# Optimization experiments

Measured on AMD Instinct MI355X. Metric: run time of the kernel, lower is better.

Reference implementation:

```python
import jax, jax.numpy as jnp
import numpy as np

B, T = 128, 32
E, H, L, V = 512, 512, 256, 16000


def setup_inputs() -> dict:
    key = jax.random.key(0)
    ks = jax.random.split(key, 12)
    u = lambda k, shape, s: jax.random.uniform(k, shape, jnp.float32, -s, s)
    kH = float(1.0 / np.sqrt(H))
    return {
        "features": jax.random.normal(ks[0], (B, E), jnp.float32),
        "captions": jax.random.randint(ks[1], (B, T), 0, V, dtype=jnp.int32),
        "lengths": jnp.full((B,), T, dtype=jnp.int32),
        "noise": jax.random.normal(ks[2], (B, T, L), jnp.float32),
        "embed_W": u(ks[3], (V, E), 0.1),
        "W_ih": u(ks[4], (4 * H, E + L), kH),
        "W_hh": u(ks[5], (4 * H, H), kH),
        "b_ih": u(ks[6], (4 * H,), kH),
        "b_hh": u(ks[7], (4 * H,), kH),
        "qz_W": u(ks[8], (2 * L, E + H), 0.1),
        "qz_b": jnp.zeros((2 * L,), jnp.float32),
        "prior_W": u(ks[9], (2 * L, H), 0.1),
        "prior_b": jnp.zeros((2 * L,), jnp.float32),
        "qx_W": u(ks[10], (V, L + H), 0.1),
        "qx_b": jnp.zeros((V,), jnp.float32),
    }


def reference(features, captions, lengths, noise, embed_W, W_ih, W_hh, b_ih, b_hh,
              qz_W, qz_b, prior_W, prior_b, qx_W, qx_b):
    def lstm_step(h, c, x):
        # PyTorch gate order: i, f, g, o
        gates = x @ W_ih.T + h @ W_hh.T + (b_ih + b_hh)
        i, f, g, o = jnp.split(gates, 4, axis=1)
        c_new = jax.nn.sigmoid(f) * c + jax.nn.sigmoid(i) * jnp.tanh(g)
        return jax.nn.sigmoid(o) * jnp.tanh(c_new), c_new

    # initial LSTM step on [features, z_0=0]
    x0 = jnp.concatenate([features, jnp.zeros((B, L), features.dtype)], axis=1)
    h, c = lstm_step(jnp.zeros((B, H), features.dtype), jnp.zeros((B, H), features.dtype), x0)

    emb = embed_W[captions]                # [B, T, E]
    emb_t = jnp.swapaxes(emb, 0, 1)        # [T, B, E]
    eps_t = jnp.swapaxes(noise, 0, 1)      # [T, B, L]

    def step(carry, xs):
        h, c = carry
        e_t, n_t = xs
        p = h @ prior_W.T + prior_b
        p_mu, p_sigma = jnp.split(p, 2, axis=1)
        q = jnp.concatenate([e_t, h], axis=1) @ qz_W.T + qz_b
        q_mu, q_sigma = jnp.split(q, 2, axis=1)
        z = n_t * q_sigma + q_mu
        logits = jnp.concatenate([z, h], axis=1) @ qx_W.T + qx_b
        q_x = jax.nn.log_softmax(logits, axis=1)
        h, c = lstm_step(h, c, jnp.concatenate([e_t, z], axis=1))
        return (h, c), (p_mu, p_sigma, q_mu, q_sigma, q_x)

    _, outs = jax.lax.scan(step, (h, c), (emb_t, eps_t))
    # pack_padded_sequence with equal lengths == time-major flatten: [T, B, D] -> [T*B, D]
    p_mus, p_sigmas, q_mus, q_sigmas, q_xs = [o.reshape((-1,) + o.shape[2:]) for o in outs]
    return ((p_mus, p_sigmas), (q_mus, q_sigmas), q_xs)
```

## Files before the change

kernel.cpp:

```cpp
#include <hip/hip_runtime.h>
#include <hip/hip_bf16.h>

typedef short bf16v8 __attribute__((ext_vector_type(8)));
typedef float f32x4 __attribute__((ext_vector_type(4)));


__device__ __forceinline__ void gload16(const void* g, void* l) {
    __builtin_amdgcn_global_load_lds(
        (const __attribute__((address_space(1))) void*)g,
        (__attribute__((address_space(3))) void*)l,
        16, 0, 0);
}

template<int SPLIT>
__global__ __launch_bounds__(256, 2) void gemm_bt(
    const __hip_bfloat16* __restrict__ A, int ldA,
    const __hip_bfloat16* __restrict__ B, int ldB,
    float* __restrict__ C, int ldC, float* __restrict__ C2,
    const float* __restrict__ bias,
    int K, int nTilesN)
{
    __shared__ __hip_bfloat16 As[128 * 32];
    __shared__ __hip_bfloat16 Bs[128 * 32];
    const int bid = blockIdx.x;
    const int bm = bid / nTilesN, bn = bid % nTilesN;
    const int m0 = bm * 128, n0 = bn * 128;
    const int tid = threadIdx.x, lane = tid & 63, wave = tid >> 6;
    const int wm = (wave & 1) * 64, wn = (wave >> 1) * 64;
    f32x4 acc[4][4] = {};

    const int ci0 = wave, ci1 = wave + 4;
    const int srow0 = ci0 * 16 + (lane >> 2);
    const int srow1 = ci1 * 16 + (lane >> 2);
    const int scol = (lane & 3) * 8;
    const __hip_bfloat16* Ag0 = A + (size_t)(m0 + srow0) * ldA + scol;
    const __hip_bfloat16* Ag1 = A + (size_t)(m0 + srow1) * ldA + scol;
    const __hip_bfloat16* Bg0 = B + (size_t)(n0 + srow0) * ldB + scol;
    const __hip_bfloat16* Bg1 = B + (size_t)(n0 + srow1) * ldB + scol;
    char* AsB = (char*)As;
    char* BsB = (char*)Bs;
    const int fr = lane & 15, k0 = (lane >> 4) * 8;

    for (int kt = 0; kt < K; kt += 32) {
        gload16(Ag0 + kt, AsB + ci0 * 1024);
        gload16(Ag1 + kt, AsB + ci1 * 1024);
        gload16(Bg0 + kt, BsB + ci0 * 1024);
        gload16(Bg1 + kt, BsB + ci1 * 1024);
        __syncthreads();
        bf16v8 a[4], b[4];
        #pragma unroll
        for (int mi = 0; mi < 4; ++mi)
            a[mi] = *(const bf16v8*)(AsB + ((wm + mi * 16 + fr) * 32 + k0) * 2);
        #pragma unroll
        for (int ni = 0; ni < 4; ++ni)
            b[ni] = *(const bf16v8*)(BsB + ((wn + ni * 16 + fr) * 32 + k0) * 2);
        #pragma unroll
        for (int mi = 0; mi < 4; ++mi)
            #pragma unroll
            for (int ni = 0; ni < 4; ++ni)
                acc[mi][ni] = __builtin_amdgcn_mfma_f32_16x16x32_bf16(a[mi], b[ni], acc[mi][ni], 0, 0, 0);
        __syncthreads();
    }
    #pragma unroll
    for (int ni = 0; ni < 4; ++ni) {
        const int n = n0 + wn + ni * 16 + fr;
        const float bv = bias ? bias[n] : 0.f;
        #pragma unroll
        for (int mi = 0; mi < 4; ++mi) {
            #pragma unroll
            for (int r = 0; r < 4; ++r) {
                const int m = m0 + wm + mi * 16 + (lane >> 4) * 4 + r;
                const float v = acc[mi][ni][r] + bv;
                if (SPLIT) {
                    if (n < 256) C[(size_t)m * 256 + n] = v;
                    else         C2[(size_t)m * 256 + (n - 256)] = v;
                } else {
                    C[(size_t)m * ldC + n] = v;
                }
            }
        }
    }
}

__global__ __launch_bounds__(256) void qz_step_k(
    const float* __restrict__ h,
    const float* __restrict__ Qe_t,
    const float* __restrict__ qz_W,
    const float* __restrict__ qz_b,
    const float* __restrict__ noise,
    float* __restrict__ out_qmu_t,
    float* __restrict__ out_qsig_t,
    float* __restrict__ zf,
    __hip_bfloat16* __restrict__ XH_z,
    int t)
{
    __shared__ float2 Wms[64][33];
    __shared__ float xt[8][32];
    const int rt = (int)blockIdx.x >> 2, nt = (int)blockIdx.x & 3;
    const int r0 = rt * 8, n0 = nt * 64;
    const int tid = threadIdx.x, lane = tid & 63, wave = tid >> 6;
    float accm[2] = {0.f, 0.f}, accs[2] = {0.f, 0.f};
    for (int kt = 0; kt < 512; kt += 32) {
        #pragma unroll
        for (int j = 0; j < 8; ++j) {
            int e = tid + j * 256, nl = e >> 5, kl = e & 31;
            size_t col = 512 + kt + kl;
            Wms[nl][kl] = make_float2(qz_W[(size_t)(n0 + nl) * 1024 + col],
                                      qz_W[(size_t)(n0 + nl + 256) * 1024 + col]);
        }
        { int rl = tid >> 5, kl = tid & 31;
          xt[rl][kl] = h[(size_t)(r0 + rl) * 512 + kt + kl]; }
        __syncthreads();
        #pragma unroll 8
        for (int kk = 0; kk < 32; ++kk) {
            float2 w = Wms[lane][kk];
            #pragma unroll
            for (int i = 0; i < 2; ++i) {
                float hv = xt[wave * 2 + i][kk];
                accm[i] = fmaf(hv, w.x, accm[i]);
                accs[i] = fmaf(hv, w.y, accs[i]);
            }
        }
        __syncthreads();
    }
    const int c = n0 + lane;
    const float bm = qz_b[c], bs = qz_b[c + 256];
    #pragma unroll
    for (int i = 0; i < 2; ++i) {
        const int b = r0 + wave * 2 + i;
        float qm = accm[i] + Qe_t[(size_t)b * 512 + c] + bm;
        float qs = accs[i] + Qe_t[(size_t)b * 512 + c + 256] + bs;
        float nz = noise[((size_t)b * 32 + t) * 256 + c];
        float z = fmaf(nz, qs, qm);
        out_qmu_t[(size_t)b * 256 + c] = qm;
        out_qsig_t[(size_t)b * 256 + c] = qs;
        zf[(size_t)b * 256 + c] = z;
        XH_z[(size_t)b * 768 + c] = __float2bfloat16(z);
    }
}

template<bool INIT>
__global__ __launch_bounds__(256) void lstm_step_k(
    const float* __restrict__ xz, const float* __restrict__ hin,
    const float* __restrict__ cin,
    const float* __restrict__ W_ih, const float* __restrict__ W_hh,
    const float* __restrict__ b_ih, const float* __restrict__ b_hh,
    const float* __restrict__ Ge,
    float* __restrict__ hout, float* __restrict__ cout,
    __hip_bfloat16* __restrict__ XH_h)
{
    __shared__ float4 Wt4[64][33];
    __shared__ float xt[8][32];
    const int rt = (int)blockIdx.x >> 3, jt = (int)blockIdx.x & 7;
    const int r0 = rt * 8, j0 = jt * 64;
    const int tid = threadIdx.x, lane = tid & 63, wave = tid >> 6;
    float acc[4][2] = {};
    const int Kz = INIT ? 512 : 256;
    const int koff = INIT ? 0 : 512;
    for (int kt = 0; kt < Kz; kt += 32) {
        #pragma unroll
        for (int j = 0; j < 8; ++j) {
            int e = tid + j * 256, nl = e >> 5, kl = e & 31;
            size_t col = (size_t)koff + kt + kl;
            Wt4[nl][kl] = make_float4(
                W_ih[(size_t)(j0 + nl) * 768 + col],
                W_ih[(size_t)(j0 + nl + 512) * 768 + col],
                W_ih[(size_t)(j0 + nl + 1024) * 768 + col],
                W_ih[(size_t)(j0 + nl + 1536) * 768 + col]);
        }
        { int rl = tid >> 5, kl = tid & 31;
          xt[rl][kl] = xz[(size_t)(r0 + rl) * Kz + kt + kl]; }
        __syncthreads();
        #pragma unroll 8
        for (int kk = 0; kk < 32; ++kk) {
            float4 w = Wt4[lane][kk];
            #pragma unroll
            for (int i = 0; i < 2; ++i) {
                float xv = xt[wave * 2 + i][kk];
                acc[0][i] = fmaf(xv, w.x, acc[0][i]);
                acc[1][i] = fmaf(xv, w.y, acc[1][i]);
                acc[2][i] = fmaf(xv, w.z, acc[2][i]);
                acc[3][i] = fmaf(xv, w.w, acc[3][i]);
            }
        }
        __syncthreads();
    }
    if constexpr (!INIT) {
        for (int kt = 0; kt < 512; kt += 32) {
            #pragma unroll
            for (int j = 0; j < 8; ++j) {
                int e = tid + j * 256, nl = e >> 5, kl = e & 31;
                size_t col = (size_t)kt + kl;
                Wt4[nl][kl] = make_float4(
                    W_hh[(size_t)(j0 + nl) * 512 + col],
                    W_hh[(size_t)(j0 + nl + 512) * 512 + col],
                    W_hh[(size_t)(j0 + nl + 1024) * 512 + col],
                    W_hh[(size_t)(j0 + nl + 1536) * 512 + col]);
            }
            { int rl = tid >> 5, kl = tid & 31;
              xt[rl][kl] = hin[(size_t)(r0 + rl) * 512 + kt + kl]; }
            __syncthreads();
            #pragma unroll 8
            for (int kk = 0; kk < 32; ++kk) {
                float4 w = Wt4[lane][kk];
                #pragma unroll
                for (int i = 0; i < 2; ++i) {
                    float xv = xt[wave * 2 + i][kk];
                    acc[0][i] = fmaf(xv, w.x, acc[0][i]);
                    acc[1][i] = fmaf(xv, w.y, acc[1][i]);
                    acc[2][i] = fmaf(xv, w.z, acc[2][i]);
                    acc[3][i] = fmaf(xv, w.w, acc[3][i]);
                }
            }
            __syncthreads();
        }
    }
    const int jj = j0 + lane;
    #pragma unroll
    for (int i = 0; i < 2; ++i) {
        const int b = r0 + wave * 2 + i;
        float g0 = acc[0][i] + b_ih[jj] + b_hh[jj];
        float g1 = acc[1][i] + b_ih[jj + 512] + b_hh[jj + 512];
        float g2 = acc[2][i] + b_ih[jj + 1024] + b_hh[jj + 1024];
        float g3 = acc[3][i] + b_ih[jj + 1536] + b_hh[jj + 1536];
        if constexpr (!INIT) {
            const float* ge = Ge + (size_t)b * 2048;
            g0 += ge[jj]; g1 += ge[jj + 512]; g2 += ge[jj + 1024]; g3 += ge[jj + 1536];
        }
        float si = 1.f / (1.f + __expf(-g0));
        float sf = 1.f / (1.f + __expf(-g1));
        float tg = tanhf(g2);
        float so = 1.f / (1.f + __expf(-g3));
        float cold = INIT ? 0.f : cin[(size_t)b * 512 + jj];
        float cn = sf * cold + si * tg;
        float hn = so * tanhf(cn);
        cout[(size_t)b * 512 + jj] = cn;
        hout[(size_t)b * 512 + jj] = hn;
        XH_h[(size_t)b * 768 + jj] = __float2bfloat16(hn);
    }
}

__global__ void embed_k(const float* __restrict__ embW, const int* __restrict__ cap,
                        __hip_bfloat16* __restrict__ Emb) {
    const int row = blockIdx.x;
    const int t = row >> 7, b = row & 127;
    const int tok = cap[b * 32 + t];
    const float* src = embW + (size_t)tok * 512;
    __hip_bfloat16* dst = Emb + (size_t)row * 512;
    for (int k = threadIdx.x; k < 512; k += blockDim.x)
        dst[k] = __float2bfloat16(src[k]);
}

__global__ void conv_lin_k(const float* __restrict__ s, __hip_bfloat16* __restrict__ d, int n) {
    for (int i = blockIdx.x * blockDim.x + threadIdx.x; i < n; i += gridDim.x * blockDim.x)
        d[i] = __float2bfloat16(s[i]);
}

__global__ void conv_s512_k(const float* __restrict__ s, int ld, __hip_bfloat16* __restrict__ d, int n) {
    for (int i = blockIdx.x * blockDim.x + threadIdx.x; i < n; i += gridDim.x * blockDim.x) {
        int r = i >> 9, c = i & 511;
        d[i] = __float2bfloat16(s[(size_t)r * ld + c]);
    }
}

__global__ __launch_bounds__(256) void lse_k(float* __restrict__ logits) {
    __shared__ float buf[16000];
    __shared__ float red[4];
    const int row = blockIdx.x;
    const int tid = threadIdx.x;
    float* p = logits + (size_t)row * 16000;
    float mx = -3.4e38f;
    for (int i = tid; i < 16000; i += 256) { float v = p[i]; buf[i] = v; mx = fmaxf(mx, v); }
    #pragma unroll
    for (int o = 32; o; o >>= 1) mx = fmaxf(mx, __shfl_xor(mx, o));
    if ((tid & 63) == 0) red[tid >> 6] = mx;
    __syncthreads();
    mx = fmaxf(fmaxf(red[0], red[1]), fmaxf(red[2], red[3]));
    float s = 0.f;
    for (int i = tid; i < 16000; i += 256) s += __expf(buf[i] - mx);
    #pragma unroll
    for (int o = 32; o; o >>= 1) s += __shfl_xor(s, o);
    __syncthreads();
    if ((tid & 63) == 0) red[tid >> 6] = s;
    __syncthreads();
    const float lse = mx + logf(red[0] + red[1] + red[2] + red[3]);
    for (int i = tid; i < 16000; i += 256) p[i] = buf[i] - lse;
}

extern "C" void kernel_launch(void* const* d_in, const int* in_sizes, int n_in,
                              void* d_out, int out_size, void* d_ws, size_t ws_size,
                              hipStream_t stream) {
    const float* features = (const float*)d_in[0];
    const int*   captions = (const int*)d_in[1];
    const float* noise    = (const float*)d_in[3];
    const float* embed_W  = (const float*)d_in[4];
    const float* W_ih     = (const float*)d_in[5];
    const float* W_hh     = (const float*)d_in[6];
    const float* b_ih     = (const float*)d_in[7];
    const float* b_hh     = (const float*)d_in[8];
    const float* qz_W     = (const float*)d_in[9];
    const float* qz_b     = (const float*)d_in[10];
    const float* prior_W  = (const float*)d_in[11];
    const float* prior_b  = (const float*)d_in[12];
    const float* qx_W     = (const float*)d_in[13];
    const float* qx_b     = (const float*)d_in[14];

    float* out0 = (float*)d_out;
    float* out1 = out0 + 4096 * 256;
    float* out2 = out1 + 4096 * 256;
    float* out3 = out2 + 4096 * 256;
    float* out4 = out3 + 4096 * 256;

    char* ws = (char*)d_ws;
    __hip_bfloat16* qxWb  = (__hip_bfloat16*)(ws + 0);
    __hip_bfloat16* Emb   = (__hip_bfloat16*)(ws + 24576000);
    __hip_bfloat16* WihEb = (__hip_bfloat16*)(ws + 28770304);
    __hip_bfloat16* qzWEb = (__hip_bfloat16*)(ws + 30867456);
    __hip_bfloat16* priWb = (__hip_bfloat16*)(ws + 31391744);
    __hip_bfloat16* XH    = (__hip_bfloat16*)(ws + 31916032);
    float* Ge  = (float*)(ws + 38404096);
    float* Qe  = (float*)(ws + 71958528);
    float* hb0 = (float*)(ws + 80347136);
    float* hb1 = (float*)(ws + 80609280);
    float* cb0 = (float*)(ws + 80871424);
    float* cb1 = (float*)(ws + 81133568);
    float* zf  = (float*)(ws + 81395712);

    conv_lin_k<<<2048, 256, 0, stream>>>(qx_W, qxWb, 16000 * 768);
    conv_lin_k<<<256, 256, 0, stream>>>(prior_W, priWb, 512 * 512);
    conv_s512_k<<<1024, 256, 0, stream>>>(W_ih, 768, WihEb, 2048 * 512);
    conv_s512_k<<<256, 256, 0, stream>>>(qz_W, 1024, qzWEb, 512 * 512);
    embed_k<<<4096, 256, 0, stream>>>(embed_W, captions, Emb);

    gemm_bt<0><<<512, 256, 0, stream>>>(Emb, 512, WihEb, 512, Ge, 2048, nullptr, nullptr, 512, 16);
    gemm_bt<0><<<128, 256, 0, stream>>>(Emb, 512, qzWEb, 512, Qe, 512, nullptr, nullptr, 512, 4);

    lstm_step_k<true><<<128, 256, 0, stream>>>(features, nullptr, nullptr, W_ih, W_hh,
                                               b_ih, b_hh, nullptr, hb0, cb0, XH + 256);

    for (int t = 0; t < 32; ++t) {
        float* hcur = (t & 1) ? hb1 : hb0;
        float* hnxt = (t & 1) ? hb0 : hb1;
        float* ccur = (t & 1) ? cb1 : cb0;
        float* cnxt = (t & 1) ? cb0 : cb1;
        qz_step_k<<<64, 256, 0, stream>>>(hcur, Qe + (size_t)t * 128 * 512, qz_W, qz_b, noise,
                                          out2 + (size_t)t * 128 * 256,
                                          out3 + (size_t)t * 128 * 256,
                                          zf, XH + (size_t)t * 128 * 768, t);
        lstm_step_k<false><<<128, 256, 0, stream>>>(zf, hcur, ccur, W_ih, W_hh, b_ih, b_hh,
                                                    Ge + (size_t)t * 128 * 2048, hnxt, cnxt,
                                                    XH + (size_t)(t + 1) * 128 * 768 + 256);
    }

    gemm_bt<1><<<128, 256, 0, stream>>>(XH + 256, 768, priWb, 512, out0, 256, out1, prior_b, 512, 4);
    gemm_bt<0><<<4000, 256, 0, stream>>>(XH, 768, qxWb, 768, out4, 16000, nullptr, qx_b, 768, 125);
    lse_k<<<4096, 256, 0, stream>>>(out4);
}
```

Measured before the change: 3.039 ms.

## Run recurrent qz and LSTM steps as bf16 MFMA GEMMs with fused epilogues

Replaces the fp32 scalar-FMA per-step qz and LSTM kernels with a bf16 MFMA GEMM kernel. Its epilogue computes z, and the LSTM gates and cell update, directly from interleaved weight rows that are prepared once up front. Biases are folded into the precomputed embedding GEMMs, and Ge is staged in the logits output buffer to save workspace. The log-softmax kernel is rewritten to hold each row in registers with 1024 threads and float4 accesses, and the qx GEMM grid is rounded to 128 N tiles with an early exit past the last column. The cost is that the recurrent state now passes through bf16, which may shift accuracy, and each step launches only 4 or 16 blocks.

```diff
diff --git a/kernel.cpp b/kernel.cpp
--- a/kernel.cpp
+++ b/kernel.cpp
@@ -11,6 +11,8 @@
         (__attribute__((address_space(3))) void*)l,
         16, 0, 0);
 }
+
+__device__ __forceinline__ float sigm(float x) { return 1.f / (1.f + __expf(-x)); }
 
 template<int SPLIT>
 __global__ __launch_bounds__(256, 2) void gemm_bt(
@@ -18,13 +20,14 @@
     const __hip_bfloat16* __restrict__ B, int ldB,
     float* __restrict__ C, int ldC, float* __restrict__ C2,
     const float* __restrict__ bias,
-    int K, int nTilesN)
+    int K, int nTilesN, int nMax)
 {
     __shared__ __hip_bfloat16 As[128 * 32];
     __shared__ __hip_bfloat16 Bs[128 * 32];
     const int bid = blockIdx.x;
     const int bm = bid / nTilesN, bn = bid % nTilesN;
     const int m0 = bm * 128, n0 = bn * 128;
+    if (n0 >= nMax) return;
     const int tid = threadIdx.x, lane = tid & 63, wave = tid >> 6;
     const int wm = (wave & 1) * 64, wn = (wave >> 1) * 64;
     f32x4 acc[4][4] = {};
@@ -82,162 +85,139 @@
     }
 }
 
-__global__ __launch_bounds__(256) void qz_step_k(
-    const float* __restrict__ h,
-    const float* __restrict__ Qe_t,
-    const float* __restrict__ qz_W,
-    const float* __restrict__ qz_b,
-    const float* __restrict__ noise,
-    float* __restrict__ out_qmu_t,
-    float* __restrict__ out_qsig_t,
-    float* __restrict__ zf,
-    __hip_bfloat16* __restrict__ XH_z,
-    int t)
+template<int EPI, bool INIT>
+__global__ __launch_bounds__(256, 2) void rec_gemm(
+    const __hip_bfloat16* __restrict__ A, int ldA,
+    const __hip_bfloat16* __restrict__ B, int K,
+    const float* __restrict__ bias,
+    const float* __restrict__ Qe_t, const float* __restrict__ noise_t,
+    float* __restrict__ qmu_out, float* __restrict__ qsig_out,
+    __hip_bfloat16* __restrict__ z_out,
+    const float* __restrict__ Ge_t,
+    const float* __restrict__ cin, float* __restrict__ cout,
+    __hip_bfloat16* __restrict__ h_out)
 {
-    __shared__ float2 Wms[64][33];
-    __shared__ float xt[8][32];
-    const int rt = (int)blockIdx.x >> 2, nt = (int)blockIdx.x & 3;
-    const int r0 = rt * 8, n0 = nt * 64;
+    __shared__ __hip_bfloat16 As[128 * 32];
+    __shared__ __hip_bfloat16 Bs[128 * 32];
+    const int n0 = blockIdx.x * 128;
     const int tid = threadIdx.x, lane = tid & 63, wave = tid >> 6;
-    float accm[2] = {0.f, 0.f}, accs[2] = {0.f, 0.f};
-    for (int kt = 0; kt < 512; kt += 32) {
-        #pragma unroll
-        for (int j = 0; j < 8; ++j) {
-            int e = tid + j * 256, nl = e >> 5, kl = e & 31;
-            size_t col = 512 + kt + kl;
-            Wms[nl][kl] = make_float2(qz_W[(size_t)(n0 + nl) * 1024 + col],
-                                      qz_W[(size_t)(n0 + nl + 256) * 1024 + col]);
-        }
-        { int rl = tid >> 5, kl = tid & 31;
-          xt[rl][kl] = h[(size_t)(r0 + rl) * 512 + kt + kl]; }
+    const int wm = (wave & 1) * 64, wn = (wave >> 1) * 64;
+    f32x4 acc[4][4] = {};
+
+    const int ci0 = wave, ci1 = wave + 4;
+    const int srow0 = ci0 * 16 + (lane >> 2);
+    const int srow1 = ci1 * 16 + (lane >> 2);
+    const int scol = (lane & 3) * 8;
+    const __hip_bfloat16* Ag0 = A + (size_t)srow0 * ldA + scol;
+    const __hip_bfloat16* Ag1 = A + (size_t)srow1 * ldA + scol;
+    const __hip_bfloat16* Bg0 = B + (size_t)(n0 + srow0) * K + scol;
+    const __hip_bfloat16* Bg1 = B + (size_t)(n0 + srow1) * K + scol;
+    char* AsB = (char*)As;
+    char* BsB = (char*)Bs;
+    const int fr = lane & 15, k0 = (lane >> 4) * 8;
+
+    for (int kt = 0; kt < K; kt += 32) {
+        gload16(Ag0 + kt, AsB + ci0 * 1024);
+        gload16(Ag1 + kt, AsB + ci1 * 1024);
+        gload16(Bg0 + kt, BsB + ci0 * 1024);
+        gload16(Bg1 + kt, BsB + ci1 * 1024);
         __syncthreads();
-        #pragma unroll 8
-        for (int kk = 0; kk < 32; ++kk) {
-            float2 w = Wms[lane][kk];
-            #pragma unroll
-            for (int i = 0; i < 2; ++i) {
-                float hv = xt[wave * 2 + i][kk];
-                accm[i] = fmaf(hv, w.x, accm[i]);
-                accs[i] = fmaf(hv, w.y, accs[i]);
+        bf16v8 a[4], b[4];
+        #pragma unroll
+        for (int mi = 0; mi < 4; ++mi)
+            a[mi] = *(const bf16v8*)(AsB + ((wm + mi * 16 + fr) * 32 + k0) * 2);
+        #pragma unroll
+        for (int ni = 0; ni < 4; ++ni)
+            b[ni] = *(const bf16v8*)(BsB + ((wn + ni * 16 + fr) * 32 + k0) * 2);
+        #pragma unroll
+        for (int mi = 0; mi < 4; ++mi)
+            #pragma unroll
+            for (int ni = 0; ni < 4; ++ni)
+                acc[mi][ni] = __builtin_amdgcn_mfma_f32_16x16x32_bf16(a[mi], b[ni], acc[mi][ni], 0, 0, 0);
+        __syncthreads();
+    }
+
+    const int rbase = (lane >> 4) * 4;
+    if constexpr (EPI == 0) {
+        #pragma unroll
+        for (int ni = 0; ni < 4; ++ni) {
+            const int n = n0 + wn + ni * 16 + fr;
+            const int j = n >> 1;
+            #pragma unroll
+            for (int mi = 0; mi < 4; ++mi) {
+                #pragma unroll
+                for (int r = 0; r < 4; ++r) {
+                    const int m = wm + mi * 16 + rbase + r;
+                    float v = acc[mi][ni][r] + Qe_t[(size_t)m * 512 + n];
+                    float o = __shfl_xor(v, 1);
+                    if ((n & 1) == 0) {
+                        float z = fmaf(noise_t[(size_t)m * 8192 + j], o, v);
+                        qmu_out[(size_t)m * 256 + j] = v;
+                        z_out[(size_t)m * 768 + j] = __float2bfloat16(z);
+                    } else {
+                        qsig_out[(size_t)m * 256 + j] = v;
+                    }
+                }
             }
         }
-        __syncthreads();
-    }
-    const int c = n0 + lane;
-    const float bm = qz_b[c], bs = qz_b[c + 256];
-    #pragma unroll
-    for (int i = 0; i < 2; ++i) {
-        const int b = r0 + wave * 2 + i;
-        float qm = accm[i] + Qe_t[(size_t)b * 512 + c] + bm;
-        float qs = accs[i] + Qe_t[(size_t)b * 512 + c + 256] + bs;
-        float nz = noise[((size_t)b * 32 + t) * 256 + c];
-        float z = fmaf(nz, qs, qm);
-        out_qmu_t[(size_t)b * 256 + c] = qm;
-        out_qsig_t[(size_t)b * 256 + c] = qs;
-        zf[(size_t)b * 256 + c] = z;
-        XH_z[(size_t)b * 768 + c] = __float2bfloat16(z);
-    }
-}
-
-template<bool INIT>
-__global__ __launch_bounds__(256) void lstm_step_k(
-    const float* __restrict__ xz, const float* __restrict__ hin,
-    const float* __restrict__ cin,
-    const float* __restrict__ W_ih, const float* __restrict__ W_hh,
-    const float* __restrict__ b_ih, const float* __restrict__ b_hh,
-    const float* __restrict__ Ge,
-    float* __restrict__ hout, float* __restrict__ cout,
-    __hip_bfloat16* __restrict__ XH_h)
-{
-    __shared__ float4 Wt4[64][33];
-    __shared__ float xt[8][32];
-    const int rt = (int)blockIdx.x >> 3, jt = (int)blockIdx.x & 7;
-    const int r0 = rt * 8, j0 = jt * 64;
-    const int tid = threadIdx.x, lane = tid & 63, wave = tid >> 6;
-    float acc[4][2] = {};
-    const int Kz = INIT ? 512 : 256;
-    const int koff = INIT ? 0 : 512;
-    for (int kt = 0; kt < Kz; kt += 32) {
-        #pragma unroll
-        for (int j = 0; j < 8; ++j) {
-            int e = tid + j * 256, nl = e >> 5, kl = e & 31;
-            size_t col = (size_t)koff + kt + kl;
-            Wt4[nl][kl] = make_float4(
-                W_ih[(size_t)(j0 + nl) * 768 + col],
-                W_ih[(size_t)(j0 + nl + 512) * 768 + col],
-                W_ih[(size_t)(j0 + nl + 1024) * 768 + col],
-                W_ih[(size_t)(j0 + nl + 1536) * 768 + col]);
-        }
-        { int rl = tid >> 5, kl = tid & 31;
-          xt[rl][kl] = xz[(size_t)(r0 + rl) * Kz + kt + kl]; }
-        __syncthreads();
-        #pragma unroll 8
-        for (int kk = 0; kk < 32; ++kk) {
-            float4 w = Wt4[lane][kk];
-            #pragma unroll
-            for (int i = 0; i < 2; ++i) {
-                float xv = xt[wave * 2 + i][kk];
-                acc[0][i] = fmaf(xv, w.x, acc[0][i]);
-                acc[1][i] = fmaf(xv, w.y, acc[1][i]);
-                acc[2][i] = fmaf(xv, w.z, acc[2][i]);
-                acc[3][i] = fmaf(xv, w.w, acc[3][i]);
+    } else {
+        #pragma unroll
+        for (int ni = 0; ni < 4; ++ni) {
+            const int n = n0 + wn + ni * 16 + fr;
+            const int j = n >> 2, g = n & 3;
+            const float bv = INIT ? bias[n] : 0.f;
+            #pragma unroll
+            for (int mi = 0; mi < 4; ++mi) {
+                #pragma unroll
+                for (int r = 0; r < 4; ++r) {
+                    const int m = wm + mi * 16 + rbase + r;
+                    float v = acc[mi][ni][r] + bv;
+                    if constexpr (!INIT) v += Ge_t[(size_t)m * 2048 + n];
+                    float x1 = __shfl_xor(v, 1);
+                    float x2 = __shfl_xor(v, 2);
+                    float x3 = __shfl_xor(v, 3);
+                    if (g == 0) {
+                        float si = sigm(v), sf = sigm(x1);
+                        float tg = tanhf(x2), so = sigm(x3);
+                        float cold = INIT ? 0.f : cin[(size_t)m * 512 + j];
+                        float cn = fmaf(sf, cold, si * tg);
+                        float hn = so * tanhf(cn);
+                        cout[(size_t)m * 512 + j] = cn;
+                        h_out[(size_t)m * 768 + j] = __float2bfloat16(hn);
+                    }
+                }
             }
         }
-        __syncthreads();
-    }
-    if constexpr (!INIT) {
-        for (int kt = 0; kt < 512; kt += 32) {
-            #pragma unroll
-            for (int j = 0; j < 8; ++j) {
-                int e = tid + j * 256, nl = e >> 5, kl = e & 31;
-                size_t col = (size_t)kt + kl;
-                Wt4[nl][kl] = make_float4(
-                    W_hh[(size_t)(j0 + nl) * 512 + col],
-                    W_hh[(size_t)(j0 + nl + 512) * 512 + col],
-                    W_hh[(size_t)(j0 + nl + 1024) * 512 + col],
-                    W_hh[(size_t)(j0 + nl + 1536) * 512 + col]);
-            }
-            { int rl = tid >> 5, kl = tid & 31;
-              xt[rl][kl] = hin[(size_t)(r0 + rl) * 512 + kt + kl]; }
-            __syncthreads();
-            #pragma unroll 8
-            for (int kk = 0; kk < 32; ++kk) {
-                float4 w = Wt4[lane][kk];
-                #pragma unroll
-                for (int i = 0; i < 2; ++i) {
-                    float xv = xt[wave * 2 + i][kk];
-                    acc[0][i] = fmaf(xv, w.x, acc[0][i]);
-                    acc[1][i] = fmaf(xv, w.y, acc[1][i]);
-                    acc[2][i] = fmaf(xv, w.z, acc[2][i]);
-                    acc[3][i] = fmaf(xv, w.w, acc[3][i]);
-                }
-            }
-            __syncthreads();
-        }
-    }
-    const int jj = j0 + lane;
-    #pragma unroll
-    for (int i = 0; i < 2; ++i) {
-        const int b = r0 + wave * 2 + i;
-        float g0 = acc[0][i] + b_ih[jj] + b_hh[jj];
-        float g1 = acc[1][i] + b_ih[jj + 512] + b_hh[jj + 512];
-        float g2 = acc[2][i] + b_ih[jj + 1024] + b_hh[jj + 1024];
-        float g3 = acc[3][i] + b_ih[jj + 1536] + b_hh[jj + 1536];
-        if constexpr (!INIT) {
-            const float* ge = Ge + (size_t)b * 2048;
-            g0 += ge[jj]; g1 += ge[jj + 512]; g2 += ge[jj + 1024]; g3 += ge[jj + 1536];
-        }
-        float si = 1.f / (1.f + __expf(-g0));
-        float sf = 1.f / (1.f + __expf(-g1));
-        float tg = tanhf(g2);
-        float so = 1.f / (1.f + __expf(-g3));
-        float cold = INIT ? 0.f : cin[(size_t)b * 512 + jj];
-        float cn = sf * cold + si * tg;
-        float hn = so * tanhf(cn);
-        cout[(size_t)b * 512 + jj] = cn;
-        hout[(size_t)b * 512 + jj] = hn;
-        XH_h[(size_t)b * 768 + jj] = __float2bfloat16(hn);
-    }
+    }
+}
+
+__global__ void prep_lstm_k(const float* __restrict__ W_ih, const float* __restrict__ W_hh,
+                            const float* __restrict__ b_ih, const float* __restrict__ b_hh,
+                            __hip_bfloat16* __restrict__ wihE, __hip_bfloat16* __restrict__ wcat,
+                            float* __restrict__ bias_comb) {
+    const int r = blockIdx.x;
+    const int j = r >> 2, g = r & 3;
+    const int src = g * 512 + j;
+    for (int c = threadIdx.x; c < 512; c += 256) {
+        wihE[(size_t)r * 512 + c] = __float2bfloat16(W_ih[(size_t)src * 768 + c]);
+        wcat[(size_t)r * 768 + 256 + c] = __float2bfloat16(W_hh[(size_t)src * 512 + c]);
+    }
+    { int c = threadIdx.x & 255;
+      if (c < 256) wcat[(size_t)r * 768 + c] = __float2bfloat16(W_ih[(size_t)src * 768 + 512 + c]); }
+    if (threadIdx.x == 0) bias_comb[r] = b_ih[src] + b_hh[src];
+}
+
+__global__ void prep_qz_k(const float* __restrict__ qz_W, const float* __restrict__ qz_b,
+                          __hip_bfloat16* __restrict__ qzwE, __hip_bfloat16* __restrict__ qzw2,
+                          float* __restrict__ qzb_i) {
+    const int r = blockIdx.x;
+    const int j = r >> 1, s = r & 1;
+    const int src = s * 256 + j;
+    for (int c = threadIdx.x; c < 512; c += 256) {
+        qzwE[(size_t)r * 512 + c] = __float2bfloat16(qz_W[(size_t)src * 1024 + c]);
+        qzw2[(size_t)r * 512 + c] = __float2bfloat16(qz_W[(size_t)src * 1024 + 512 + c]);
+    }
+    if (threadIdx.x == 0) qzb_i[r] = qz_b[src];
 }
 
 __global__ void embed_k(const float* __restrict__ embW, const int* __restrict__ cap,
@@ -256,35 +236,53 @@
         d[i] = __float2bfloat16(s[i]);
 }
 
-__global__ void conv_s512_k(const float* __restrict__ s, int ld, __hip_bfloat16* __restrict__ d, int n) {
-    for (int i = blockIdx.x * blockDim.x + threadIdx.x; i < n; i += gridDim.x * blockDim.x) {
-        int r = i >> 9, c = i & 511;
-        d[i] = __float2bfloat16(s[(size_t)r * ld + c]);
-    }
-}
-
-__global__ __launch_bounds__(256) void lse_k(float* __restrict__ logits) {
-    __shared__ float buf[16000];
-    __shared__ float red[4];
-    const int row = blockIdx.x;
-    const int tid = threadIdx.x;
+__global__ __launch_bounds__(1024) void lse_k(float* __restrict__ logits) {
+    __shared__ float redm[16], reds[16];
+    const int row = blockIdx.x, tid = threadIdx.x;
     float* p = logits + (size_t)row * 16000;
+    const bool full = (tid < 928);
+    float4 v[4];
     float mx = -3.4e38f;
-    for (int i = tid; i < 16000; i += 256) { float v = p[i]; buf[i] = v; mx = fmaxf(mx, v); }
+    #pragma unroll
+    for (int c = 0; c < 3; ++c) {
+        v[c] = *(const float4*)(p + c * 4096 + tid * 4);
+        mx = fmaxf(mx, fmaxf(fmaxf(v[c].x, v[c].y), fmaxf(v[c].z, v[c].w)));
+    }
+    if (full) {
+        v[3] = *(const float4*)(p + 12288 + tid * 4);
+        mx = fmaxf(mx, fmaxf(fmaxf(v[3].x, v[3].y), fmaxf(v[3].z, v[3].w)));
+    }
     #pragma unroll
     for (int o = 32; o; o >>= 1) mx = fmaxf(mx, __shfl_xor(mx, o));
-    if ((tid & 63) == 0) red[tid >> 6] = mx;
+    if ((tid & 63) == 0) redm[tid >> 6] = mx;
     __syncthreads();
-    mx = fmaxf(fmaxf(red[0], red[1]), fmaxf(red[2], red[3]));
+    #pragma unroll
+    for (int i = 0; i < 16; ++i) mx = fmaxf(mx, redm[i]);
     float s = 0.f;
-    for (int i = tid; i < 16000; i += 256) s += __expf(buf[i] - mx);
+    #pragma unroll
+    for (int c = 0; c < 3; ++c)
+        s += __expf(v[c].x - mx) + __expf(v[c].y - mx) + __expf(v[c].z - mx) + __expf(v[c].w - mx);
+    if (full)
+        s += __expf(v[3].x - mx) + __expf(v[3].y - mx) + __expf(v[3].z - mx) + __expf(v[3].w - mx);
     #pragma unroll
     for (int o = 32; o; o >>= 1) s += __shfl_xor(s, o);
+    if ((tid & 63) == 0) reds[tid >> 6] = s;
     __syncthreads();
-    if ((tid & 63) == 0) red[tid >> 6] = s;
-    __syncthreads();
-    const float lse = mx + logf(red[0] + red[1] + red[2] + red[3]);
-    for (int i = tid; i < 16000; i += 256) p[i] = buf[i] - lse;
+    float tot = 0.f;
+    #pragma unroll
+    for (int i = 0; i < 16; ++i) tot += reds[i];
+    const float lse = mx + logf(tot);
+    #pragma unroll
+    for (int c = 0; c < 3; ++c) {
+        float4 w = v[c];
+        w.x -= lse; w.y -= lse; w.z -= lse; w.w -= lse;
+        *(float4*)(p + c * 4096 + tid * 4) = w;
+    }
+    if (full) {
+        float4 w = v[3];
+        w.x -= lse; w.y -= lse; w.z -= lse; w.w -= lse;
+        *(float4*)(p + 12288 + tid * 4) = w;
+    }
 }
 
 extern "C" void kernel_launch(void* const* d_in, const int* in_sizes, int n_in,
@@ -312,47 +310,54 @@
     float* out4 = out3 + 4096 * 256;
 
     char* ws = (char*)d_ws;
-    __hip_bfloat16* qxWb  = (__hip_bfloat16*)(ws + 0);
-    __hip_bfloat16* Emb   = (__hip_bfloat16*)(ws + 24576000);
-    __hip_bfloat16* WihEb = (__hip_bfloat16*)(ws + 28770304);
-    __hip_bfloat16* qzWEb = (__hip_bfloat16*)(ws + 30867456);
-    __hip_bfloat16* priWb = (__hip_bfloat16*)(ws + 31391744);
-    __hip_bfloat16* XH    = (__hip_bfloat16*)(ws + 31916032);
-    float* Ge  = (float*)(ws + 38404096);
-    float* Qe  = (float*)(ws + 71958528);
-    float* hb0 = (float*)(ws + 80347136);
-    float* hb1 = (float*)(ws + 80609280);
-    float* cb0 = (float*)(ws + 80871424);
-    float* cb1 = (float*)(ws + 81133568);
-    float* zf  = (float*)(ws + 81395712);
+    __hip_bfloat16* qxWb   = (__hip_bfloat16*)(ws + 0);
+    __hip_bfloat16* Emb    = (__hip_bfloat16*)(ws + 24576000);
+    __hip_bfloat16* wihE   = (__hip_bfloat16*)(ws + 28770304);
+    __hip_bfloat16* wcat   = (__hip_bfloat16*)(ws + 30867456);
+    __hip_bfloat16* qzwE   = (__hip_bfloat16*)(ws + 34013184);
+    __hip_bfloat16* qzw2   = (__hip_bfloat16*)(ws + 34537472);
+    __hip_bfloat16* priWb  = (__hip_bfloat16*)(ws + 35061760);
+    __hip_bfloat16* featb  = (__hip_bfloat16*)(ws + 35586048);
+    __hip_bfloat16* XH     = (__hip_bfloat16*)(ws + 35717120);
+    float* qzb_i     = (float*)(ws + 42205184);
+    float* bias_comb = (float*)(ws + 42207232);
+    float* cb0       = (float*)(ws + 42215424);
+    float* cb1       = (float*)(ws + 42477568);
+    float* Qe        = (float*)(ws + 42739712);
+    float* Ge        = out4;
 
     conv_lin_k<<<2048, 256, 0, stream>>>(qx_W, qxWb, 16000 * 768);
     conv_lin_k<<<256, 256, 0, stream>>>(prior_W, priWb, 512 * 512);
-    conv_s512_k<<<1024, 256, 0, stream>>>(W_ih, 768, WihEb, 2048 * 512);
-    conv_s512_k<<<256, 256, 0, stream>>>(qz_W, 1024, qzWEb, 512 * 512);
+    conv_lin_k<<<64, 256, 0, stream>>>(features, featb, 128 * 512);
+    prep_lstm_k<<<2048, 256, 0, stream>>>(W_ih, W_hh, b_ih, b_hh, wihE, wcat, bias_comb);
+    prep_qz_k<<<512, 256, 0, stream>>>(qz_W, qz_b, qzwE, qzw2, qzb_i);
     embed_k<<<4096, 256, 0, stream>>>(embed_W, captions, Emb);
 
-    gemm_bt<0><<<512, 256, 0, stream>>>(Emb, 512, WihEb, 512, Ge, 2048, nullptr, nullptr, 512, 16);
-    gemm_bt<0><<<128, 256, 0, stream>>>(Emb, 512, qzWEb, 512, Qe, 512, nullptr, nullptr, 512, 4);
-
-    lstm_step_k<true><<<128, 256, 0, stream>>>(features, nullptr, nullptr, W_ih, W_hh,
-                                               b_ih, b_hh, nullptr, hb0, cb0, XH + 256);
+    gemm_bt<0><<<512, 256, 0, stream>>>(Emb, 512, wihE, 512, Ge, 2048, nullptr, bias_comb, 512, 16, 1 << 30);
+    gemm_bt<0><<<128, 256, 0, stream>>>(Emb, 512, qzwE, 512, Qe, 512, nullptr, qzb_i, 512, 4, 1 << 30);
+
+    rec_gemm<1, true><<<16, 256, 0, stream>>>(
+        featb, 512, wihE, 512, bias_comb,
+        nullptr, nullptr, nullptr, nullptr, nullptr,
+        nullptr, nullptr, cb0, XH + 256);
 
     for (int t = 0; t < 32; ++t) {
-        float* hcur = (t & 1) ? hb1 : hb0;
-        float* hnxt = (t & 1) ? hb0 : hb1;
         float* ccur = (t & 1) ? cb1 : cb0;
         float* cnxt = (t & 1) ? cb0 : cb1;
-        qz_step_k<<<64, 256, 0, stream>>>(hcur, Qe + (size_t)t * 128 * 512, qz_W, qz_b, noise,
-                                          out2 + (size_t)t * 128 * 256,
-                                          out3 + (size_t)t * 128 * 256,
-                                          zf, XH + (size_t)t * 128 * 768, t);
-        lstm_step_k<false><<<128, 256, 0, stream>>>(zf, hcur, ccur, W_ih, W_hh, b_ih, b_hh,
-                                                    Ge + (size_t)t * 128 * 2048, hnxt, cnxt,
-                                                    XH + (size_t)(t + 1) * 128 * 768 + 256);
-    }
-
-    gemm_bt<1><<<128, 256, 0, stream>>>(XH + 256, 768, priWb, 512, out0, 256, out1, prior_b, 512, 4);
-    gemm_bt<0><<<4000, 256, 0, stream>>>(XH, 768, qxWb, 768, out4, 16000, nullptr, qx_b, 768, 125);
-    lse_k<<<4096, 256, 0, stream>>>(out4);
-}
+        __hip_bfloat16* slot = XH + (size_t)t * 98304;
+        rec_gemm<0, false><<<4, 256, 0, stream>>>(
+            slot + 256, 768, qzw2, 512, nullptr,
+            Qe + (size_t)t * 128 * 512, noise + (size_t)t * 256,
+            out2 + (size_t)t * 128 * 256, out3 + (size_t)t * 128 * 256, slot,
+            nullptr, nullptr, nullptr, nullptr);
+        rec_gemm<1, false><<<16, 256, 0, stream>>>(
+            slot, 768, wcat, 768, nullptr,
+            nullptr, nullptr, nullptr, nullptr, nullptr,
+            Ge + (size_t)t * 128 * 2048, ccur, cnxt,
+            XH + (size_t)(t + 1) * 98304 + 256);
+    }
+
+    gemm_bt<1><<<128, 256, 0, stream>>>(XH + 256, 768, priWb, 512, out0, 256, out1, prior_b, 512, 4, 1 << 30);
+    gemm_bt<0><<<4096, 256, 0, stream>>>(XH, 768, qxWb, 768, out4, 16000, nullptr, qx_b, 768, 128, 16000);
+    lse_k<<<4096, 1024, 0, stream>>>(out4);
+}
```

Result: slower. 3.981 ms (+31.0%).
